# Performance work log

Hardware: AMD Instinct MI355X
Metric: run time of the kernel (lower is better)

## Reference

```python
import jax, jax.numpy as jnp
import numpy as np

F_DIM = 128        # feature_dim
LATENT = 256       # latent_dim
HEADS = 4          # n_head
N_GRAPHS = 256
NODES_PER = 100    # < 180 (pos table size)
N = N_GRAPHS * NODES_PER
DEG = 8
E = N * DEG
MAX_POS = 180
NEG_SLOPE = 0.2


def sinusoid_table(n_node, d):
    pos = np.arange(n_node, dtype=np.float64)[:, None]
    j = np.arange(d, dtype=np.float64)[None, :]
    ang = pos / np.power(10000.0, 2.0 * (np.floor(j / 2.0)) / d)
    ang[:, 0::2] = np.sin(ang[:, 0::2])
    ang[:, 1::2] = np.cos(ang[:, 1::2])
    return jnp.asarray(ang, dtype=jnp.float32)  # [n_node, d]


def gat_layer(x, src, dst, W, a_src, a_dst, bias):
    # x: [N, in], W: [in, H*C], a_src/a_dst: [H, C], bias: [H*C]
    H, C = a_src.shape
    xl = (x @ W).reshape(N, H, C)                      # [N,H,C]
    s = jnp.einsum('nhc,hc->nh', xl, a_src)            # [N,H]
    d = jnp.einsum('nhc,hc->nh', xl, a_dst)            # [N,H]
    e = jax.nn.leaky_relu(s[src] + d[dst], NEG_SLOPE)  # [E,H]
    emax = jax.ops.segment_max(e, dst, num_segments=N)
    ex = jnp.exp(e - emax[dst])
    den = jax.ops.segment_sum(ex, dst, num_segments=N)
    alpha = ex / (den[dst] + 1e-16)                    # [E,H]
    out = jax.ops.segment_sum(alpha[:, :, None] * xl[src], dst, num_segments=N)
    return out.reshape(N, H * C) + bias


def setup_inputs() -> dict:
    key = jax.random.key(0)
    ks = jax.random.split(key, 20)
    sc = 0.05
    z = jax.random.normal(ks[0], (N_GRAPHS, LATENT), dtype=jnp.float32)
    batch = jnp.repeat(jnp.arange(N_GRAPHS, dtype=jnp.int64), NODES_PER)
    base = (jnp.arange(N, dtype=jnp.int64) // NODES_PER) * NODES_PER
    nbr = jax.random.randint(ks[1], (N, DEG), 0, NODES_PER, dtype=jnp.int64)
    src = (base[:, None] + nbr).reshape(-1)
    dst = jnp.repeat(jnp.arange(N, dtype=jnp.int64), DEG)
    edge_index = jnp.stack([src, dst], 0)
    HF = HEADS * F_DIM
    p = {
        'W0': jax.random.normal(ks[2], (LATENT, F_DIM)) * sc,
        'b0': jnp.zeros((F_DIM,), jnp.float32),
        'W1': jax.random.normal(ks[3], (2 * F_DIM, HF)) * sc,
        'as1': jax.random.normal(ks[4], (HEADS, F_DIM)) * sc,
        'ad1': jax.random.normal(ks[5], (HEADS, F_DIM)) * sc,
        'b1': jnp.zeros((HF,), jnp.float32),
        'W2': jax.random.normal(ks[6], (HF, HF)) * sc,
        'as2': jax.random.normal(ks[7], (HEADS, F_DIM)) * sc,
        'ad2': jax.random.normal(ks[8], (HEADS, F_DIM)) * sc,
        'b2': jnp.zeros((HF,), jnp.float32),
        'W3': jax.random.normal(ks[9], (HF, HF)) * sc,
        'as3': jax.random.normal(ks[10], (HEADS, F_DIM)) * sc,
        'ad3': jax.random.normal(ks[11], (HEADS, F_DIM)) * sc,
        'b3': jnp.zeros((HF,), jnp.float32),
        'Wg': jax.random.normal(ks[12], (HF, F_DIM)) * sc,
        'bg': jnp.zeros((F_DIM,), jnp.float32),
        'Wf': jax.random.normal(ks[13], (F_DIM, 5)) * sc,
        'bf': jnp.zeros((5,), jnp.float32),
    }
    return {'z': z, 'edge_index': edge_index, 'batch': batch, **p}


def reference(z, edge_index, batch, W0, b0, W1, as1, ad1, b1,
              W2, as2, ad2, b2, W3, as3, ad3, b3, Wg, bg, Wf, bf):
    # node order within each graph (intended semantics of node_order_within_batch)
    counts = jax.ops.segment_sum(jnp.ones((N,), jnp.int32), batch, num_segments=N_GRAPHS)
    cum = jnp.concatenate([jnp.zeros((1,), jnp.int32), jnp.cumsum(counts)[:-1]])
    order = jnp.arange(N, dtype=jnp.int32) - cum[batch]
    pos = sinusoid_table(MAX_POS, F_DIM)[order]        # [N, F]  (detached buffer)

    h = (z @ W0 + b0)[batch]                           # [N, F]
    h = jax.nn.relu(jnp.concatenate([h, pos], axis=1)) # [N, 2F]

    # PyG GATConv default add_self_loops=True
    loop = jnp.arange(N, dtype=edge_index.dtype)
    src = jnp.concatenate([edge_index[0], loop])
    dst = jnp.concatenate([edge_index[1], loop])

    h = jax.nn.relu(gat_layer(h, src, dst, W1, as1, ad1, b1))
    h = jax.nn.relu(gat_layer(h, src, dst, W2, as2, ad2, b2))
    h = jax.nn.relu(gat_layer(h, src, dst, W3, as3, ad3, b3))
    h = jax.nn.relu(h @ Wg + bg)
    return h @ Wf + bf                                 # [N, 5]
```

## Files before the change

kernel.cpp:

```cpp
#include <hip/hip_runtime.h>
#include <hip/hip_bf16.h>
#include <math.h>

#define N_GRAPHS 256
#define NODES_PER 100
#define NN (N_GRAPHS * NODES_PER)
#define DEG 8
#define FD 128
#define LAT 256
#define HFD 512
#define NEG_SLOPE 0.2f

typedef _Float16 half8 __attribute__((ext_vector_type(8)));
typedef float float4v __attribute__((ext_vector_type(4)));

__device__ __forceinline__ int xcd_swz(int bid, int total) {
    int q = total >> 3;
    return (bid & 7) * q + (bid >> 3);
}

__device__ __forceinline__ void gload_lds16(const _Float16* g, _Float16* l) {
    __builtin_amdgcn_global_load_lds(
        (const __attribute__((address_space(1))) unsigned int*)g,
        (__attribute__((address_space(3))) unsigned int*)l, 16, 0, 0);
}

__global__ void g0_kernel(const float* __restrict__ z, const float* __restrict__ W0,
                          const float* __restrict__ b0, float* __restrict__ g0) {
    __shared__ float s_z[LAT];
    int g = blockIdx.x;
    int j = threadIdx.x;
    s_z[j]       = z[g * LAT + j];
    s_z[j + 128] = z[g * LAT + 128 + j];
    __syncthreads();
    float acc = 0.f;
    #pragma unroll 8
    for (int k = 0; k < LAT; ++k)
        acc += s_z[k] * W0[k * FD + j];
    g0[g * FD + j] = acc + b0[j];
}

__global__ void build_x1_kernel(const float* __restrict__ g0,
                                const int* __restrict__ batch, _Float16* __restrict__ x1) {
    __shared__ int s_b, s_ord;
    int i = blockIdx.x;
    int t = threadIdx.x;
    if (t == 0) {
        int b = batch[i];
        int lo = 0, hi = i;
        while (lo < hi) { int mid = (lo + hi) >> 1; if (batch[mid] < b) lo = mid + 1; else hi = mid; }
        s_b = b;
        s_ord = i - lo;
    }
    __syncthreads();
    float v;
    if (t < 128) {
        v = g0[s_b * FD + t];
    } else {
        int j = t - 128;
        int j2 = j >> 1;
        float freq = expf(-(float)j2 * 0.1439115683f);
        float ang = (float)s_ord * freq;
        v = (j & 1) ? cosf(ang) : sinf(ang);
    }
    x1[(size_t)i * 256 + t] = (_Float16)fmaxf(v, 0.f);
}

__global__ void wconv_all_kernel(const float* __restrict__ W1, const float* __restrict__ W2,
                                 const float* __restrict__ W3, const float* __restrict__ Wg,
                                 _Float16* __restrict__ W1t, _Float16* __restrict__ W2t,
                                 _Float16* __restrict__ W3t, _Float16* __restrict__ Wgt) {
    __shared__ float tile[32][33];
    int b = blockIdx.x;
    const float* in; _Float16* out; int K, Nw, tid2;
    if (b < 128)      { in = W1; out = W1t; K = 256; Nw = 512; tid2 = b; }
    else if (b < 384) { in = W2; out = W2t; K = 512; Nw = 512; tid2 = b - 128; }
    else if (b < 640) { in = W3; out = W3t; K = 512; Nw = 512; tid2 = b - 384; }
    else              { in = Wg; out = Wgt; K = 512; Nw = 128; tid2 = b - 640; }
    int nxt = Nw / 32;
    int nb = (tid2 % nxt) * 32, kb = (tid2 / nxt) * 32;
    int tx = threadIdx.x & 31, ty = threadIdx.x >> 5;
    #pragma unroll
    for (int r = 0; r < 4; ++r)
        tile[ty + 8 * r][tx] = in[(size_t)(kb + ty + 8 * r) * Nw + nb + tx];
    __syncthreads();
    #pragma unroll
    for (int r = 0; r < 4; ++r)
        out[(size_t)(nb + ty + 8 * r) * K + kb + tx] = (_Float16)tile[tx][ty + 8 * r];
}

template <int MODE>
__global__ __launch_bounds__(256) void hgemm_kernel(
    const _Float16* __restrict__ X,
    const _Float16* __restrict__ Wt,
    const float* __restrict__ bias,
    const float* __restrict__ a_src,
    const float* __restrict__ a_dst,
    float* __restrict__ sbuf,
    float* __restrict__ dbuf,
    const float* __restrict__ Wf,
    const float* __restrict__ bfv,
    void* __restrict__ Yv,
    int K, int ldy, int nbx) {
    __shared__ __align__(16) _Float16 As[128 * 32];
    __shared__ __align__(16) _Float16 Bs[128 * 32];
    __shared__ float red[5][128][2];
    const int lin = xcd_swz(blockIdx.x, gridDim.x);
    const int row0 = (lin / nbx) * 128;
    const int col0 = (lin % nbx) * 128;
    const int tid  = threadIdx.x;
    const int lane = tid & 63;
    const int wave = tid >> 6;
    const int wm = wave >> 1;
    const int wn = wave & 1;

    const int srow = tid >> 2;
    const int sq   = (tid & 3) ^ ((tid >> 3) & 3);
    const _Float16* gA0 = X  + (size_t)(row0 + srow) * K + sq * 8;
    const _Float16* gB0 = Wt + (size_t)(col0 + srow) * K + sq * 8;
    const _Float16* gA1 = gA0 + (size_t)64 * K;
    const _Float16* gB1 = gB0 + (size_t)64 * K;
    _Float16* ldsA0 = &As[wave * 512];
    _Float16* ldsA1 = &As[2048 + wave * 512];
    _Float16* ldsB0 = &Bs[wave * 512];
    _Float16* ldsB1 = &Bs[2048 + wave * 512];

    const int kq  = lane >> 4;
    const int l15 = lane & 15;

    float4v acc[4][4];
    #pragma unroll
    for (int i = 0; i < 4; ++i)
        #pragma unroll
        for (int j = 0; j < 4; ++j)
            acc[i][j] = (float4v){0.f, 0.f, 0.f, 0.f};

    const int nk = K >> 5;
    for (int ks = 0; ks < nk; ++ks) {
        gload_lds16(gA0 + ks * 32, ldsA0);
        gload_lds16(gA1 + ks * 32, ldsA1);
        gload_lds16(gB0 + ks * 32, ldsB0);
        gload_lds16(gB1 + ks * 32, ldsB1);
        __syncthreads();
        half8 af[4], bfr[4];
        #pragma unroll
        for (int mi = 0; mi < 4; ++mi) {
            int r = wm * 64 + mi * 16 + l15;
            af[mi] = *(const half8*)&As[r * 32 + ((kq ^ ((r >> 1) & 3)) * 8)];
        }
        #pragma unroll
        for (int ni = 0; ni < 4; ++ni) {
            int c = wn * 64 + ni * 16 + l15;
            bfr[ni] = *(const half8*)&Bs[c * 32 + ((kq ^ ((c >> 1) & 3)) * 8)];
        }
        #pragma unroll
        for (int mi = 0; mi < 4; ++mi)
            #pragma unroll
            for (int ni = 0; ni < 4; ++ni)
                acc[mi][ni] = __builtin_amdgcn_mfma_f32_16x16x32_f16(af[mi], bfr[ni], acc[mi][ni], 0, 0, 0);
        __syncthreads();
    }

    if (MODE == 0) {
        const int h = col0 >> 7;
        float asv[4], adv[4];
        #pragma unroll
        for (int ni = 0; ni < 4; ++ni) {
            int ch = wn * 64 + ni * 16 + l15;
            asv[ni] = a_src[h * FD + ch];
            adv[ni] = a_dst[h * FD + ch];
        }
        #pragma unroll
        for (int mi = 0; mi < 4; ++mi) {
            int rb = row0 + wm * 64 + mi * 16 + ((lane >> 4) << 2);
            #pragma unroll
            for (int j = 0; j < 4; ++j) {
                float ps = 0.f, pd = 0.f;
                #pragma unroll
                for (int ni = 0; ni < 4; ++ni) {
                    float v = acc[mi][ni][j];
                    int c = col0 + wn * 64 + ni * 16 + l15;
                    ((_Float16*)Yv)[(size_t)(rb + j) * ldy + c] = (_Float16)v;
                    ps += v * asv[ni];
                    pd += v * adv[ni];
                }
                #pragma unroll
                for (int m = 8; m >= 1; m >>= 1) {
                    ps += __shfl_xor(ps, m);
                    pd += __shfl_xor(pd, m);
                }
                if (l15 == 0) {
                    int rloc = wm * 64 + mi * 16 + ((lane >> 4) << 2) + j;
                    red[0][rloc][wn] = ps;
                    red[1][rloc][wn] = pd;
                }
            }
        }
        __syncthreads();
        if (tid < 128) {
            sbuf[(size_t)(row0 + tid) * 4 + h] = red[0][tid][0] + red[0][tid][1];
            dbuf[(size_t)(row0 + tid) * 4 + h] = red[1][tid][0] + red[1][tid][1];
        }
    } else {
        float bgv[4], wf[4][5];
        #pragma unroll
        for (int ni = 0; ni < 4; ++ni) {
            int c = wn * 64 + ni * 16 + l15;
            bgv[ni] = bias[c];
            #pragma unroll
            for (int q = 0; q < 5; ++q) wf[ni][q] = Wf[c * 5 + q];
        }
        #pragma unroll
        for (int mi = 0; mi < 4; ++mi) {
            #pragma unroll
            for (int j = 0; j < 4; ++j) {
                float vr[4];
                #pragma unroll
                for (int ni = 0; ni < 4; ++ni)
                    vr[ni] = fmaxf(acc[mi][ni][j] + bgv[ni], 0.f);
                #pragma unroll
                for (int q = 0; q < 5; ++q) {
                    float p = vr[0] * wf[0][q] + vr[1] * wf[1][q] + vr[2] * wf[2][q] + vr[3] * wf[3][q];
                    #pragma unroll
                    for (int m = 8; m >= 1; m >>= 1) p += __shfl_xor(p, m);
                    if (l15 == 0) {
                        int rloc = wm * 64 + mi * 16 + ((lane >> 4) << 2) + j;
                        red[q][rloc][wn] = p;
                    }
                }
            }
        }
        __syncthreads();
        if (tid < 128) {
            float* o = (float*)Yv;
            #pragma unroll
            for (int q = 0; q < 5; ++q)
                o[(size_t)(row0 + tid) * 5 + q] = red[q][tid][0] + red[q][tid][1] + bfv[q];
        }
    }
}

__global__ void agg_kernel(const _Float16* __restrict__ xl,
                           const float* __restrict__ s, const float* __restrict__ d,
                           const int* __restrict__ esrc,
                           const float* __restrict__ bias,
                           _Float16* __restrict__ xout) {
    int wave = threadIdx.x >> 6;
    int lane = threadIdx.x & 63;
    int blk = xcd_swz(blockIdx.x, gridDim.x);
    int i = blk * 4 + wave;
    int h = lane >> 4;

    int sk = (lane < 8) ? esrc[i * DEG + lane] : i;
    int srcs[9];
    #pragma unroll
    for (int k = 0; k < 9; ++k) srcs[k] = __shfl(sk, k);

    float dh = d[i * 4 + h];
    float e[9];
    float m = -1e30f;
    #pragma unroll
    for (int k = 0; k < 9; ++k) {
        float v = s[srcs[k] * 4 + h] + dh;
        v = (v >= 0.f) ? v : NEG_SLOPE * v;
        e[k] = v;
        m = fmaxf(m, v);
    }
    float den = 0.f;
    #pragma unroll
    for (int k = 0; k < 9; ++k) { e[k] = __expf(e[k] - m); den += e[k]; }
    float inv = 1.f / (den + 1e-16f);

    int c0 = lane * 8;
    float acc[8] = {};
    #pragma unroll
    for (int k = 0; k < 9; ++k) {
        half8 x = *(const half8*)&xl[(size_t)srcs[k] * HFD + c0];
        float a = e[k] * inv;
        #pragma unroll
        for (int j = 0; j < 8; ++j) acc[j] += a * (float)x[j];
    }
    float4v b0 = *(const float4v*)&bias[c0];
    float4v b1 = *(const float4v*)&bias[c0 + 4];
    half8 o;
    #pragma unroll
    for (int j = 0; j < 4; ++j) {
        o[j]     = (_Float16)fmaxf(acc[j] + b0[j], 0.f);
        o[j + 4] = (_Float16)fmaxf(acc[j + 4] + b1[j], 0.f);
    }
    *(half8*)&xout[(size_t)i * HFD + c0] = o;
}

extern "C" void kernel_launch(void* const* d_in, const int* in_sizes, int n_in,
                              void* d_out, int out_size, void* d_ws, size_t ws_size,
                              hipStream_t stream) {
    const float* z    = (const float*)d_in[0];
    const int*  eidx  = (const int*)d_in[1];
    const int*  batch = (const int*)d_in[2];
    const float* W0  = (const float*)d_in[3];
    const float* b0  = (const float*)d_in[4];
    const float* W1  = (const float*)d_in[5];
    const float* as1 = (const float*)d_in[6];
    const float* ad1 = (const float*)d_in[7];
    const float* b1  = (const float*)d_in[8];
    const float* W2  = (const float*)d_in[9];
    const float* as2 = (const float*)d_in[10];
    const float* ad2 = (const float*)d_in[11];
    const float* b2  = (const float*)d_in[12];
    const float* W3  = (const float*)d_in[13];
    const float* as3 = (const float*)d_in[14];
    const float* ad3 = (const float*)d_in[15];
    const float* b3  = (const float*)d_in[16];
    const float* Wg  = (const float*)d_in[17];
    const float* bg  = (const float*)d_in[18];
    const float* Wf  = (const float*)d_in[19];
    const float* bfv = (const float*)d_in[20];
    float* out = (float*)d_out;

    float* ws   = (float*)d_ws;
    float* g0   = ws;
    float* sbuf = g0 + 32768;
    float* dbuf = sbuf + (size_t)NN * 4;
    _Float16* Yh  = (_Float16*)(dbuf + (size_t)NN * 4);
    _Float16* Xh  = Yh + (size_t)NN * 512;
    _Float16* W1t = Xh + (size_t)NN * 512;
    _Float16* W2t = W1t + 512 * 256;
    _Float16* W3t = W2t + 512 * 512;
    _Float16* Wgt = W3t + 512 * 512;

    g0_kernel<<<N_GRAPHS, FD, 0, stream>>>(z, W0, b0, g0);
    build_x1_kernel<<<NN, 256, 0, stream>>>(g0, batch, Xh);
    wconv_all_kernel<<<704, 256, 0, stream>>>(W1, W2, W3, Wg, W1t, W2t, W3t, Wgt);

    const int nbL = (NN / 128) * (HFD / 128);
    const int nbH = (NN / 128) * (FD / 128);

    hgemm_kernel<0><<<nbL, 256, 0, stream>>>(Xh, W1t, nullptr, as1, ad1, sbuf, dbuf, nullptr, nullptr, Yh, 256, HFD, HFD / 128);
    agg_kernel<<<NN / 4, 256, 0, stream>>>(Yh, sbuf, dbuf, eidx, b1, Xh);

    hgemm_kernel<0><<<nbL, 256, 0, stream>>>(Xh, W2t, nullptr, as2, ad2, sbuf, dbuf, nullptr, nullptr, Yh, 512, HFD, HFD / 128);
    agg_kernel<<<NN / 4, 256, 0, stream>>>(Yh, sbuf, dbuf, eidx, b2, Xh);

    hgemm_kernel<0><<<nbL, 256, 0, stream>>>(Xh, W3t, nullptr, as3, ad3, sbuf, dbuf, nullptr, nullptr, Yh, 512, HFD, HFD / 128);
    agg_kernel<<<NN / 4, 256, 0, stream>>>(Yh, sbuf, dbuf, eidx, b3, Xh);

    hgemm_kernel<1><<<nbH, 256, 0, stream>>>(Xh, Wgt, bg, nullptr, nullptr, nullptr, nullptr, Wf, bfv, out, 512, 5, FD / 128);
}
```

Measured before the change: 306.9 us.

## Fuse GAT projection GEMM and attention aggregation into one per-graph kernel

Replaces the separate projection GEMM and edge-aggregation kernels with one kernel per graph. Each block computes the 100-node projection for all 512 columns, keeps it in LDS with an XOR swizzle, reduces the attention logits in LDS, and runs the softmax aggregation from LDS. This removes the global write and gather-read of the projected features and the s/d buffers, and cuts the launch count. The costs are only 256 large blocks with about 120KB of LDS each, no double buffering, and the weight operand read straight from global memory (L2) by every block, so GEMM efficiency and occupancy may drop.

```diff
diff --git a/kernel.cpp b/kernel.cpp
--- a/kernel.cpp
+++ b/kernel.cpp
@@ -89,35 +89,177 @@
         out[(size_t)(nb + ty + 8 * r) * K + kb + tx] = (_Float16)tile[tx][ty + 8 * r];
 }
 
-template <int MODE>
-__global__ __launch_bounds__(256) void hgemm_kernel(
+template <int K>
+__global__ __launch_bounds__(512, 2) void gat_fused_kernel(
+    const _Float16* __restrict__ X,
+    const _Float16* __restrict__ Wt,
+    const float* __restrict__ a_src,
+    const float* __restrict__ a_dst,
+    const int* __restrict__ esrc,
+    const float* __restrict__ bias,
+    _Float16* __restrict__ Xout) {
+    __shared__ __align__(16) _Float16 As[128 * 32];
+    __shared__ __align__(16) _Float16 Ylds[100 * 512];
+    __shared__ float sdpart[112][8][2];
+    __shared__ float s_lds[112][4];
+    __shared__ float d_lds[112][4];
+
+    const int g    = blockIdx.x;
+    const int tid  = threadIdx.x;
+    const int lane = tid & 63;
+    const int wc   = tid >> 6;
+    const int kq   = lane >> 4;
+    const int l15  = lane & 15;
+    const int rowbase = g * NODES_PER;
+
+    const int srow = tid >> 2;
+    const int sq   = (tid & 3) ^ ((tid >> 3) & 3);
+    const _Float16* gA = X + (size_t)(rowbase + srow) * K + sq * 8;
+    _Float16* ldsA = &As[wc * 512];
+
+    const _Float16* gW[4];
+    #pragma unroll
+    for (int ni = 0; ni < 4; ++ni) {
+        int c = wc * 64 + ni * 16 + l15;
+        gW[ni] = Wt + (size_t)c * K + kq * 8;
+    }
+
+    float4v acc[7][4];
+    #pragma unroll
+    for (int mi = 0; mi < 7; ++mi)
+        #pragma unroll
+        for (int ni = 0; ni < 4; ++ni)
+            acc[mi][ni] = (float4v){0.f, 0.f, 0.f, 0.f};
+
+    const int nk = K >> 5;
+    for (int ks = 0; ks < nk; ++ks) {
+        gload_lds16(gA + ks * 32, ldsA);
+        half8 bfr[4];
+        #pragma unroll
+        for (int ni = 0; ni < 4; ++ni)
+            bfr[ni] = *(const half8*)(gW[ni] + ks * 32);
+        __syncthreads();
+        half8 af[7];
+        #pragma unroll
+        for (int mi = 0; mi < 7; ++mi) {
+            int r = mi * 16 + l15;
+            af[mi] = *(const half8*)&As[r * 32 + ((kq ^ ((r >> 1) & 3)) * 8)];
+        }
+        #pragma unroll
+        for (int mi = 0; mi < 7; ++mi)
+            #pragma unroll
+            for (int ni = 0; ni < 4; ++ni)
+                acc[mi][ni] = __builtin_amdgcn_mfma_f32_16x16x32_f16(af[mi], bfr[ni], acc[mi][ni], 0, 0, 0);
+        __syncthreads();
+    }
+
+    float asv[4], adv[4];
+    #pragma unroll
+    for (int ni = 0; ni < 4; ++ni) {
+        int c = wc * 64 + ni * 16 + l15;
+        asv[ni] = a_src[c];
+        adv[ni] = a_dst[c];
+    }
+    const int hi4 = lane >> 4;
+    #pragma unroll
+    for (int mi = 0; mi < 7; ++mi) {
+        #pragma unroll
+        for (int j = 0; j < 4; ++j) {
+            int r = mi * 16 + hi4 * 4 + j;
+            float ps = 0.f, pd = 0.f;
+            #pragma unroll
+            for (int ni = 0; ni < 4; ++ni) {
+                float v = acc[mi][ni][j];
+                ps += v * asv[ni];
+                pd += v * adv[ni];
+                if (r < NODES_PER) {
+                    int c = wc * 64 + ni * 16 + l15;
+                    Ylds[r * 512 + (((c >> 3) ^ (r & 7)) * 8) + (c & 7)] = (_Float16)v;
+                }
+            }
+            #pragma unroll
+            for (int m = 8; m >= 1; m >>= 1) {
+                ps += __shfl_xor(ps, m);
+                pd += __shfl_xor(pd, m);
+            }
+            if (l15 == 0) {
+                sdpart[r][wc][0] = ps;
+                sdpart[r][wc][1] = pd;
+            }
+        }
+    }
+    __syncthreads();
+    if (tid < 448) {
+        int r = tid >> 2, h = tid & 3;
+        s_lds[r][h] = sdpart[r][2 * h][0] + sdpart[r][2 * h + 1][0];
+        d_lds[r][h] = sdpart[r][2 * h][1] + sdpart[r][2 * h + 1][1];
+    }
+    __syncthreads();
+
+    const int hd = lane >> 4;
+    const int c0 = lane * 8;
+    float4v b0 = *(const float4v*)&bias[c0];
+    float4v b1 = *(const float4v*)&bias[c0 + 4];
+    for (int i = wc; i < NODES_PER; i += 8) {
+        int sg = (lane < 8) ? (esrc[(size_t)(rowbase + i) * DEG + lane] - rowbase) : i;
+        int sl[9];
+        #pragma unroll
+        for (int k = 0; k < 9; ++k) sl[k] = __shfl(sg, k);
+        float dh = d_lds[i][hd];
+        float e[9];
+        float mx = -1e30f;
+        #pragma unroll
+        for (int k = 0; k < 9; ++k) {
+            float v = s_lds[sl[k]][hd] + dh;
+            v = (v >= 0.f) ? v : NEG_SLOPE * v;
+            e[k] = v;
+            mx = fmaxf(mx, v);
+        }
+        float den = 0.f;
+        #pragma unroll
+        for (int k = 0; k < 9; ++k) { e[k] = __expf(e[k] - mx); den += e[k]; }
+        float inv = 1.f / (den + 1e-16f);
+        float a8[8] = {};
+        #pragma unroll
+        for (int k = 0; k < 9; ++k) {
+            half8 y = *(const half8*)&Ylds[sl[k] * 512 + ((lane ^ (sl[k] & 7)) * 8)];
+            float a = e[k] * inv;
+            #pragma unroll
+            for (int j = 0; j < 8; ++j) a8[j] += a * (float)y[j];
+        }
+        half8 o;
+        #pragma unroll
+        for (int j = 0; j < 4; ++j) {
+            o[j]     = (_Float16)fmaxf(a8[j] + b0[j], 0.f);
+            o[j + 4] = (_Float16)fmaxf(a8[j + 4] + b1[j], 0.f);
+        }
+        *(half8*)&Xout[(size_t)(rowbase + i) * HFD + c0] = o;
+    }
+}
+
+__global__ __launch_bounds__(256) void head_kernel(
     const _Float16* __restrict__ X,
     const _Float16* __restrict__ Wt,
     const float* __restrict__ bias,
-    const float* __restrict__ a_src,
-    const float* __restrict__ a_dst,
-    float* __restrict__ sbuf,
-    float* __restrict__ dbuf,
     const float* __restrict__ Wf,
     const float* __restrict__ bfv,
-    void* __restrict__ Yv,
-    int K, int ldy, int nbx) {
+    float* __restrict__ out) {
     __shared__ __align__(16) _Float16 As[128 * 32];
     __shared__ __align__(16) _Float16 Bs[128 * 32];
     __shared__ float red[5][128][2];
     const int lin = xcd_swz(blockIdx.x, gridDim.x);
-    const int row0 = (lin / nbx) * 128;
-    const int col0 = (lin % nbx) * 128;
+    const int row0 = lin * 128;
     const int tid  = threadIdx.x;
     const int lane = tid & 63;
     const int wave = tid >> 6;
     const int wm = wave >> 1;
     const int wn = wave & 1;
+    const int K = 512;
 
     const int srow = tid >> 2;
     const int sq   = (tid & 3) ^ ((tid >> 3) & 3);
     const _Float16* gA0 = X  + (size_t)(row0 + srow) * K + sq * 8;
-    const _Float16* gB0 = Wt + (size_t)(col0 + srow) * K + sq * 8;
+    const _Float16* gB0 = Wt + (size_t)srow * K + sq * 8;
     const _Float16* gA1 = gA0 + (size_t)64 * K;
     const _Float16* gB1 = gB0 + (size_t)64 * K;
     _Float16* ldsA0 = &As[wave * 512];
@@ -135,8 +277,7 @@
         for (int j = 0; j < 4; ++j)
             acc[i][j] = (float4v){0.f, 0.f, 0.f, 0.f};
 
-    const int nk = K >> 5;
-    for (int ks = 0; ks < nk; ++ks) {
+    for (int ks = 0; ks < 16; ++ks) {
         gload_lds16(gA0 + ks * 32, ldsA0);
         gload_lds16(gA1 + ks * 32, ldsA1);
         gload_lds16(gB0 + ks * 32, ldsB0);
@@ -161,134 +302,40 @@
         __syncthreads();
     }
 
-    if (MODE == 0) {
-        const int h = col0 >> 7;
-        float asv[4], adv[4];
-        #pragma unroll
-        for (int ni = 0; ni < 4; ++ni) {
-            int ch = wn * 64 + ni * 16 + l15;
-            asv[ni] = a_src[h * FD + ch];
-            adv[ni] = a_dst[h * FD + ch];
-        }
-        #pragma unroll
-        for (int mi = 0; mi < 4; ++mi) {
-            int rb = row0 + wm * 64 + mi * 16 + ((lane >> 4) << 2);
-            #pragma unroll
-            for (int j = 0; j < 4; ++j) {
-                float ps = 0.f, pd = 0.f;
+    float bgv[4], wf[4][5];
+    #pragma unroll
+    for (int ni = 0; ni < 4; ++ni) {
+        int c = wn * 64 + ni * 16 + l15;
+        bgv[ni] = bias[c];
+        #pragma unroll
+        for (int q = 0; q < 5; ++q) wf[ni][q] = Wf[c * 5 + q];
+    }
+    #pragma unroll
+    for (int mi = 0; mi < 4; ++mi) {
+        #pragma unroll
+        for (int j = 0; j < 4; ++j) {
+            float vr[4];
+            #pragma unroll
+            for (int ni = 0; ni < 4; ++ni)
+                vr[ni] = fmaxf(acc[mi][ni][j] + bgv[ni], 0.f);
+            #pragma unroll
+            for (int q = 0; q < 5; ++q) {
+                float p = vr[0] * wf[0][q] + vr[1] * wf[1][q] + vr[2] * wf[2][q] + vr[3] * wf[3][q];
                 #pragma unroll
-                for (int ni = 0; ni < 4; ++ni) {
-                    float v = acc[mi][ni][j];
-                    int c = col0 + wn * 64 + ni * 16 + l15;
-                    ((_Float16*)Yv)[(size_t)(rb + j) * ldy + c] = (_Float16)v;
-                    ps += v * asv[ni];
-                    pd += v * adv[ni];
-                }
-                #pragma unroll
-                for (int m = 8; m >= 1; m >>= 1) {
-                    ps += __shfl_xor(ps, m);
-                    pd += __shfl_xor(pd, m);
-                }
+                for (int m = 8; m >= 1; m >>= 1) p += __shfl_xor(p, m);
                 if (l15 == 0) {
                     int rloc = wm * 64 + mi * 16 + ((lane >> 4) << 2) + j;
-                    red[0][rloc][wn] = ps;
-                    red[1][rloc][wn] = pd;
+                    red[q][rloc][wn] = p;
                 }
             }
         }
-        __syncthreads();
-        if (tid < 128) {
-            sbuf[(size_t)(row0 + tid) * 4 + h] = red[0][tid][0] + red[0][tid][1];
-            dbuf[(size_t)(row0 + tid) * 4 + h] = red[1][tid][0] + red[1][tid][1];
-        }
-    } else {
-        float bgv[4], wf[4][5];
-        #pragma unroll
-        for (int ni = 0; ni < 4; ++ni) {
-            int c = wn * 64 + ni * 16 + l15;
-            bgv[ni] = bias[c];
-            #pragma unroll
-            for (int q = 0; q < 5; ++q) wf[ni][q] = Wf[c * 5 + q];
-        }
-        #pragma unroll
-        for (int mi = 0; mi < 4; ++mi) {
-            #pragma unroll
-            for (int j = 0; j < 4; ++j) {
-                float vr[4];
-                #pragma unroll
-                for (int ni = 0; ni < 4; ++ni)
-                    vr[ni] = fmaxf(acc[mi][ni][j] + bgv[ni], 0.f);
-                #pragma unroll
-                for (int q = 0; q < 5; ++q) {
-                    float p = vr[0] * wf[0][q] + vr[1] * wf[1][q] + vr[2] * wf[2][q] + vr[3] * wf[3][q];
-                    #pragma unroll
-                    for (int m = 8; m >= 1; m >>= 1) p += __shfl_xor(p, m);
-                    if (l15 == 0) {
-                        int rloc = wm * 64 + mi * 16 + ((lane >> 4) << 2) + j;
-                        red[q][rloc][wn] = p;
-                    }
-                }
-            }
-        }
-        __syncthreads();
-        if (tid < 128) {
-            float* o = (float*)Yv;
-            #pragma unroll
-            for (int q = 0; q < 5; ++q)
-                o[(size_t)(row0 + tid) * 5 + q] = red[q][tid][0] + red[q][tid][1] + bfv[q];
-        }
-    }
-}
-
-__global__ void agg_kernel(const _Float16* __restrict__ xl,
-                           const float* __restrict__ s, const float* __restrict__ d,
-                           const int* __restrict__ esrc,
-                           const float* __restrict__ bias,
-                           _Float16* __restrict__ xout) {
-    int wave = threadIdx.x >> 6;
-    int lane = threadIdx.x & 63;
-    int blk = xcd_swz(blockIdx.x, gridDim.x);
-    int i = blk * 4 + wave;
-    int h = lane >> 4;
-
-    int sk = (lane < 8) ? esrc[i * DEG + lane] : i;
-    int srcs[9];
-    #pragma unroll
-    for (int k = 0; k < 9; ++k) srcs[k] = __shfl(sk, k);
-
-    float dh = d[i * 4 + h];
-    float e[9];
-    float m = -1e30f;
-    #pragma unroll
-    for (int k = 0; k < 9; ++k) {
-        float v = s[srcs[k] * 4 + h] + dh;
-        v = (v >= 0.f) ? v : NEG_SLOPE * v;
-        e[k] = v;
-        m = fmaxf(m, v);
-    }
-    float den = 0.f;
-    #pragma unroll
-    for (int k = 0; k < 9; ++k) { e[k] = __expf(e[k] - m); den += e[k]; }
-    float inv = 1.f / (den + 1e-16f);
-
-    int c0 = lane * 8;
-    float acc[8] = {};
-    #pragma unroll
-    for (int k = 0; k < 9; ++k) {
-        half8 x = *(const half8*)&xl[(size_t)srcs[k] * HFD + c0];
-        float a = e[k] * inv;
-        #pragma unroll
-        for (int j = 0; j < 8; ++j) acc[j] += a * (float)x[j];
-    }
-    float4v b0 = *(const float4v*)&bias[c0];
-    float4v b1 = *(const float4v*)&bias[c0 + 4];
-    half8 o;
-    #pragma unroll
-    for (int j = 0; j < 4; ++j) {
-        o[j]     = (_Float16)fmaxf(acc[j] + b0[j], 0.f);
-        o[j + 4] = (_Float16)fmaxf(acc[j + 4] + b1[j], 0.f);
-    }
-    *(half8*)&xout[(size_t)i * HFD + c0] = o;
+    }
+    __syncthreads();
+    if (tid < 128) {
+        #pragma unroll
+        for (int q = 0; q < 5; ++q)
+            out[(size_t)(row0 + tid) * 5 + q] = red[q][tid][0] + red[q][tid][1] + bfv[q];
+    }
 }
 
 extern "C" void kernel_launch(void* const* d_in, const int* in_sizes, int n_in,
@@ -319,30 +366,21 @@
 
     float* ws   = (float*)d_ws;
     float* g0   = ws;
-    float* sbuf = g0 + 32768;
-    float* dbuf = sbuf + (size_t)NN * 4;
-    _Float16* Yh  = (_Float16*)(dbuf + (size_t)NN * 4);
-    _Float16* Xh  = Yh + (size_t)NN * 512;
-    _Float16* W1t = Xh + (size_t)NN * 512;
+    _Float16* Xh1 = (_Float16*)(g0 + 32768);
+    _Float16* Xa  = Xh1 + (size_t)NN * 256;
+    _Float16* Xb  = Xa + (size_t)NN * 512;
+    _Float16* W1t = Xb + (size_t)NN * 512;
     _Float16* W2t = W1t + 512 * 256;
     _Float16* W3t = W2t + 512 * 512;
     _Float16* Wgt = W3t + 512 * 512;
 
     g0_kernel<<<N_GRAPHS, FD, 0, stream>>>(z, W0, b0, g0);
-    build_x1_kernel<<<NN, 256, 0, stream>>>(g0, batch, Xh);
+    build_x1_kernel<<<NN, 256, 0, stream>>>(g0, batch, Xh1);
     wconv_all_kernel<<<704, 256, 0, stream>>>(W1, W2, W3, Wg, W1t, W2t, W3t, Wgt);
 
-    const int nbL = (NN / 128) * (HFD / 128);
-    const int nbH = (NN / 128) * (FD / 128);
-
-    hgemm_kernel<0><<<nbL, 256, 0, stream>>>(Xh, W1t, nullptr, as1, ad1, sbuf, dbuf, nullptr, nullptr, Yh, 256, HFD, HFD / 128);
-    agg_kernel<<<NN / 4, 256, 0, stream>>>(Yh, sbuf, dbuf, eidx, b1, Xh);
-
-    hgemm_kernel<0><<<nbL, 256, 0, stream>>>(Xh, W2t, nullptr, as2, ad2, sbuf, dbuf, nullptr, nullptr, Yh, 512, HFD, HFD / 128);
-    agg_kernel<<<NN / 4, 256, 0, stream>>>(Yh, sbuf, dbuf, eidx, b2, Xh);
-
-    hgemm_kernel<0><<<nbL, 256, 0, stream>>>(Xh, W3t, nullptr, as3, ad3, sbuf, dbuf, nullptr, nullptr, Yh, 512, HFD, HFD / 128);
-    agg_kernel<<<NN / 4, 256, 0, stream>>>(Yh, sbuf, dbuf, eidx, b3, Xh);
-
-    hgemm_kernel<1><<<nbH, 256, 0, stream>>>(Xh, Wgt, bg, nullptr, nullptr, nullptr, nullptr, Wf, bfv, out, 512, 5, FD / 128);
-}
+    gat_fused_kernel<256><<<N_GRAPHS, 512, 0, stream>>>(Xh1, W1t, as1, ad1, eidx, b1, Xa);
+    gat_fused_kernel<512><<<N_GRAPHS, 512, 0, stream>>>(Xa,  W2t, as2, ad2, eidx, b2, Xb);
+    gat_fused_kernel<512><<<N_GRAPHS, 512, 0, stream>>>(Xb,  W3t, as3, ad3, eidx, b3, Xa);
+
+    head_kernel<<<NN / 128, 256, 0, stream>>>(Xa, Wgt, bg, Wf, bfv, out);
+}
```

Measured after the change: 318.4 us. 3.7% more time.
